# Kernel tuning notes

Hardware: AMD Instinct MI355X
Metric: run time of the kernel (lower is better)

Reference implementation:

```python
import jax, jax.numpy as jnp
import numpy as np

B, S, D_MODEL, D_FF, E, K = 4, 2048, 1024, 4096, 8, 2
CAP_FACTOR = 1.0


def setup_inputs() -> dict:
    key = jax.random.key(0)
    ks = jax.random.split(key, 6)
    std = 0.02
    return {
        "x": jax.random.normal(ks[0], (B, S, D_MODEL), jnp.float32),
        "router_w": jax.random.normal(ks[1], (E, D_MODEL), jnp.float32) * std,  # Linear(d_model,E,bias=False) weight
        "w1": jax.random.normal(ks[2], (E, D_MODEL, D_FF), jnp.float32) * std,
        "b1": jnp.zeros((E, D_FF), jnp.float32),
        "w2": jax.random.normal(ks[3], (E, D_FF, D_MODEL), jnp.float32) * std,
        "b2": jnp.zeros((E, D_MODEL), jnp.float32),
    }


def reference(x, router_w, w1, b1, w2, b2):
    b, s, d = x.shape
    T = b * s
    e = router_w.shape[0]
    capacity = int(CAP_FACTOR * T / e)  # static
    xf = x.reshape(T, d)

    # --- routing ---
    logits = xf @ router_w.T                       # [T,E]
    probs = jax.nn.softmax(logits, axis=-1)
    vals, idx = jax.lax.top_k(probs, K)            # [T,K] values / expert ids
    vals = vals / vals.sum(-1, keepdims=True)

    # dense gate matrix [T,E]; top_k experts are distinct so this is a scatter of K weights per token
    ar = jnp.arange(T)
    gates = jnp.zeros((T, e), x.dtype).at[ar[:, None], idx].add(vals)

    # --- load-balancing loss ---
    counts = jnp.zeros((e,), jnp.float32).at[idx.reshape(-1)].add(1.0)
    ideal = T * K / e
    lb_loss = jnp.sum((counts - ideal) ** 2) / (T ** 2)

    # --- capacity-limited dispatch (first `capacity` tokens in token order per expert) ---
    mask = gates > 0                                               # [T,E]
    order = jnp.argsort(jnp.logical_not(mask), axis=0)[:capacity]  # stable: assigned tokens first, ascending token id -> [cap,E]
    valid = jnp.take_along_axis(mask, order, axis=0)               # [cap,E] token actually assigned & within capacity
    idx_ec = order.T                                               # [E,cap]

    # --- grouped expert MLP ---
    xg = xf[idx_ec]                                                # [E,cap,D]
    h = jax.nn.gelu(jnp.einsum('ecd,edf->ecf', xg, w1) + b1[:, None, :], approximate=False)
    y = jnp.einsum('ecf,efd->ecd', h, w2) + b2[:, None, :]         # [E,cap,D]

    # --- combine (scatter-add with routing weights; dropped/invalid slots get weight 0) ---
    wt = gates[idx_ec, jnp.arange(e)[:, None]] * valid.T           # [E,cap]
    out = jnp.zeros((T, d), x.dtype).at[idx_ec.reshape(-1)].add((y * wt[..., None]).reshape(-1, d))
    return out.reshape(b, s, d), lb_loss
```

## Files before the change

kernel.cpp:

```cpp
#include <hip/hip_runtime.h>
#include <hip/hip_bf16.h>

#define T_TOK 8192
#define DMODEL 1024
#define DFF 4096
#define NEXP 8
#define CAP 1024

typedef __attribute__((ext_vector_type(8))) __bf16 bf16x8;
typedef __attribute__((ext_vector_type(4))) float f32x4;

__device__ __forceinline__ unsigned short f2bf(float f) {
  union { float f; unsigned int u; } v;
  v.f = f;
  return (unsigned short)((v.u + 0x7fffu + ((v.u >> 16) & 1u)) >> 16);
}

__device__ __forceinline__ float fast_gelu(float v) {
  float x = fabsf(v) * 0.70710678118654752440f;
  float t = __builtin_amdgcn_rcpf(1.0f + 0.3275911f * x);
  float poly = t * (0.254829592f + t * (-0.284496736f + t * (1.421413741f +
               t * (-1.453152027f + t * 1.061405429f))));
  float er = 1.0f - poly * __expf(-x * x);
  float s = (v >= 0.0f) ? er : -er;
  return 0.5f * v * (1.0f + s);
}

__device__ __forceinline__ void load_lds16(const unsigned short* g, unsigned short* l) {
  __builtin_amdgcn_global_load_lds((const __attribute__((address_space(1))) void*)g,
                                   (__attribute__((address_space(3))) void*)l,
                                   16, 0, 0);
}

__global__ void k_router(const float* __restrict__ x, const float* __restrict__ rw,
                         unsigned short* __restrict__ xb,
                         int* __restrict__ tk_idx, float* __restrict__ tk_w) {
  int wv = threadIdx.x >> 6, lane = threadIdx.x & 63;
  int t = blockIdx.x * 4 + wv;
  const float4* xr = (const float4*)(x + (size_t)t * DMODEL);
  uint2* xbw = (uint2*)(xb + (size_t)t * DMODEL);
  float acc[NEXP];
#pragma unroll
  for (int e = 0; e < NEXP; ++e) acc[e] = 0.f;
#pragma unroll
  for (int j = 0; j < DMODEL / 256; ++j) {
    float4 v = xr[j * 64 + lane];
#pragma unroll
    for (int e = 0; e < NEXP; ++e) {
      float4 w = ((const float4*)(rw + e * DMODEL))[j * 64 + lane];
      acc[e] += v.x * w.x + v.y * w.y + v.z * w.z + v.w * w.w;
    }
    uint2 p;
    p.x = (unsigned int)f2bf(v.x) | ((unsigned int)f2bf(v.y) << 16);
    p.y = (unsigned int)f2bf(v.z) | ((unsigned int)f2bf(v.w) << 16);
    xbw[j * 64 + lane] = p;
  }
#pragma unroll
  for (int e = 0; e < NEXP; ++e)
    for (int off = 32; off; off >>= 1) acc[e] += __shfl_xor(acc[e], off);
  if (lane == 0) {
    int i0 = 0;
    for (int e = 1; e < NEXP; ++e) if (acc[e] > acc[i0]) i0 = e;
    int i1 = (i0 == 0) ? 1 : 0;
    for (int e = 0; e < NEXP; ++e) if (e != i0 && acc[e] > acc[i1]) i1 = e;
    float ex = expf(acc[i1] - acc[i0]);
    float w0 = 1.f / (1.f + ex);
    float w1 = ex / (1.f + ex);
    tk_idx[2 * t] = i0; tk_idx[2 * t + 1] = i1;
    tk_w[2 * t] = w0;  tk_w[2 * t + 1] = w1;
  }
}

__global__ void k_transpose_cvt(const float* __restrict__ src, unsigned short* __restrict__ dst,
                                int Kd, int Nd) {
  __shared__ unsigned short tile[64][73];
  int e = blockIdx.z;
  size_t k0 = (size_t)blockIdx.y * 64, n0 = (size_t)blockIdx.x * 64;
  int tid = threadIdx.x;
  const float* sb = src + (size_t)e * Kd * Nd;
  int r = tid >> 4, cg = (tid & 15) * 4;
  for (int rr = 0; rr < 4; ++rr) {
    int row = r + rr * 16;
    float4 v = *(const float4*)(sb + (k0 + row) * Nd + n0 + cg);
    tile[row][cg + 0] = f2bf(v.x);
    tile[row][cg + 1] = f2bf(v.y);
    tile[row][cg + 2] = f2bf(v.z);
    tile[row][cg + 3] = f2bf(v.w);
  }
  __syncthreads();
  unsigned short* db = dst + (size_t)e * Nd * Kd;
  int rn = tid >> 3, kg = (tid & 7) * 8;
  for (int rr = 0; rr < 2; ++rr) {
    int nrow = rn + rr * 32;
    union { unsigned short h[8]; uint4 v; } o;
#pragma unroll
    for (int j = 0; j < 8; ++j) o.h[j] = tile[kg + j][nrow];
    *(uint4*)(db + (n0 + nrow) * Kd + k0 + kg) = o.v;
  }
}

__global__ void k_scan(const int* __restrict__ tk_idx, const float* __restrict__ tk_w,
                       int* __restrict__ etok, float* __restrict__ egate,
                       float* __restrict__ loss_out) {
  __shared__ int wavecnt[16][NEXP];
  __shared__ int waveoff[16][NEXP];
  __shared__ int offs[NEXP];
  __shared__ int ctot[NEXP];
  int tid = threadIdx.x;
  int lane = tid & 63, wv = tid >> 6;
  if (tid < NEXP) offs[tid] = 0;
  for (int i = tid; i < NEXP * CAP; i += 1024) { etok[i] = 0; egate[i] = 0.f; }
  __syncthreads();
  unsigned long long lt = (1ULL << lane) - 1ULL;
  for (int c = 0; c < T_TOK / 1024; ++c) {
    int t = c * 1024 + tid;
    int e0 = tk_idx[2 * t], e1 = tk_idx[2 * t + 1];
    float w0 = tk_w[2 * t], w1 = tk_w[2 * t + 1];
    int p0 = 0, p1 = 0;
#pragma unroll
    for (int e = 0; e < NEXP; ++e) {
      unsigned long long bal = __ballot((e0 == e) || (e1 == e));
      if (e0 == e) p0 = __popcll(bal & lt);
      if (e1 == e) p1 = __popcll(bal & lt);
      if (lane == 0) wavecnt[wv][e] = __popcll(bal);
    }
    __syncthreads();
    if (tid < NEXP) {
      int s = 0;
      for (int w = 0; w < 16; ++w) { waveoff[w][tid] = s; s += wavecnt[w][tid]; }
      ctot[tid] = s;
    }
    __syncthreads();
    int r0 = offs[e0] + waveoff[wv][e0] + p0;
    int r1 = offs[e1] + waveoff[wv][e1] + p1;
    if (r0 < CAP) { etok[e0 * CAP + r0] = t; egate[e0 * CAP + r0] = w0; }
    if (r1 < CAP) { etok[e1 * CAP + r1] = t; egate[e1 * CAP + r1] = w1; }
    __syncthreads();
    if (tid < NEXP) offs[tid] += ctot[tid];
    __syncthreads();
  }
  if (tid == 0) {
    float loss = 0.f;
    for (int e = 0; e < NEXP; ++e) {
      float d = (float)offs[e] - 2048.0f;
      loss += d * d;
    }
    loss_out[0] = loss / (8192.0f * 8192.0f);
  }
}

__global__ __launch_bounds__(256) void k_gemm1(
    const unsigned short* __restrict__ xb, const unsigned short* __restrict__ w1t,
    const float* __restrict__ b1, const int* __restrict__ etok,
    unsigned short* __restrict__ H) {
  __shared__ __align__(16) unsigned short smem[8192];
  unsigned short* As = smem;
  unsigned short* Bs = smem + 4096;
  int tid = threadIdx.x;
  int lane = tid & 63, wv = tid >> 6;
  int bid = blockIdx.x;
  int e = bid >> 8;
  int b = bid & 255;
  int nl = b & 7, m = (b >> 3) & 7, nh = b >> 6;
  int m0 = m * 128, n0 = (nh * 8 + nl) * 128;

  const unsigned short* gA[2];
  const unsigned short* gB[2];
  unsigned short* lA[2];
  unsigned short* lB[2];
#pragma unroll
  for (int s = 0; s < 2; ++s) {
    int i = s * 256 + tid;
    int row = i >> 2, cb = (i & 3) * 8;
    int tok = etok[e * CAP + m0 + row];
    gA[s] = xb + (size_t)tok * DMODEL + cb;
    gB[s] = w1t + ((size_t)e * DFF + n0 + row) * DMODEL + cb;
    int wb = (s * 256 + wv * 64) * 8;
    lA[s] = As + wb;
    lB[s] = Bs + wb;
  }

  f32x4 zero = {0.f, 0.f, 0.f, 0.f};
  f32x4 acc[4][4];
#pragma unroll
  for (int mi = 0; mi < 4; ++mi)
#pragma unroll
    for (int ni = 0; ni < 4; ++ni) acc[mi][ni] = zero;

  int wm = (wv >> 1) * 64, wn = (wv & 1) * 64;
  int fr = lane & 15, quad = lane >> 4;
  const unsigned short* pa = As + (wm + fr) * 32 + quad * 8;
  const unsigned short* pb = Bs + (wn + fr) * 32 + quad * 8;

  for (int k0 = 0; k0 < DMODEL; k0 += 32) {
#pragma unroll
    for (int s = 0; s < 2; ++s) {
      load_lds16(gA[s] + k0, lA[s]);
      load_lds16(gB[s] + k0, lB[s]);
    }
    __syncthreads();
    bf16x8 av[4], bv[4];
#pragma unroll
    for (int mi = 0; mi < 4; ++mi) av[mi] = *(const bf16x8*)(pa + mi * 16 * 32);
#pragma unroll
    for (int ni = 0; ni < 4; ++ni) bv[ni] = *(const bf16x8*)(pb + ni * 16 * 32);
#pragma unroll
    for (int mi = 0; mi < 4; ++mi)
#pragma unroll
      for (int ni = 0; ni < 4; ++ni)
        acc[mi][ni] = __builtin_amdgcn_mfma_f32_16x16x32_bf16(bv[ni], av[mi], acc[mi][ni], 0, 0, 0);
    __syncthreads();
  }

  unsigned short* EP = smem + wv * 1536;
#pragma unroll
  for (int ni = 0; ni < 4; ++ni) {
    float4 b4 = *(const float4*)(b1 + e * DFF + n0 + wn + ni * 16 + quad * 4);
#pragma unroll
    for (int mi = 0; mi < 4; ++mi) {
      float v0 = fast_gelu(acc[mi][ni][0] + b4.x);
      float v1 = fast_gelu(acc[mi][ni][1] + b4.y);
      float v2 = fast_gelu(acc[mi][ni][2] + b4.z);
      float v3 = fast_gelu(acc[mi][ni][3] + b4.w);
      uint2 p;
      p.x = (unsigned int)f2bf(v0) | ((unsigned int)f2bf(v1) << 16);
      p.y = (unsigned int)f2bf(v2) | ((unsigned int)f2bf(v3) << 16);
      *(uint2*)(EP + (mi * 16 + fr) * 24 + quad * 4) = p;
    }
#pragma unroll
    for (int t = 0; t < 2; ++t) {
      int row = t * 32 + (lane >> 1), chunk = lane & 1;
      uint4 v = *(const uint4*)(EP + row * 24 + chunk * 8);
      *(uint4*)(H + ((size_t)e * CAP + m0 + wm + row) * DFF + n0 + wn + ni * 16 + chunk * 8) = v;
    }
  }
}

__global__ __launch_bounds__(256) void k_gemm2(
    const unsigned short* __restrict__ H, const unsigned short* __restrict__ w2t,
    const float* __restrict__ b2, const int* __restrict__ etok,
    const float* __restrict__ egate, float* __restrict__ out) {
  __shared__ __align__(16) unsigned short smem[8192];
  unsigned short* As = smem;
  unsigned short* Bs = smem + 4096;
  int tid = threadIdx.x;
  int lane = tid & 63, wv = tid >> 6;
  int bid = blockIdx.x;
  int e = bid >> 7;
  int ks = (bid >> 6) & 1;
  int m0 = ((bid >> 3) & 7) * 128;
  int n0 = (bid & 7) * 128;
  int kbase = ks * (DFF / 2);

  const unsigned short* gA[2];
  const unsigned short* gB[2];
  unsigned short* lA[2];
  unsigned short* lB[2];
#pragma unroll
  for (int s = 0; s < 2; ++s) {
    int i = s * 256 + tid;
    int row = i >> 2, cb = (i & 3) * 8;
    gA[s] = H + ((size_t)e * CAP + m0 + row) * DFF + kbase + cb;
    gB[s] = w2t + ((size_t)e * DMODEL + n0 + row) * DFF + kbase + cb;
    int wb = (s * 256 + wv * 64) * 8;
    lA[s] = As + wb;
    lB[s] = Bs + wb;
  }

  f32x4 zero = {0.f, 0.f, 0.f, 0.f};
  f32x4 acc[4][4];
#pragma unroll
  for (int mi = 0; mi < 4; ++mi)
#pragma unroll
    for (int ni = 0; ni < 4; ++ni) acc[mi][ni] = zero;

  int wm = (wv >> 1) * 64, wn = (wv & 1) * 64;
  int fr = lane & 15, quad = lane >> 4;
  const unsigned short* pa = As + (wm + fr) * 32 + quad * 8;
  const unsigned short* pb = Bs + (wn + fr) * 32 + quad * 8;

  for (int k0 = 0; k0 < DFF / 2; k0 += 32) {
#pragma unroll
    for (int s = 0; s < 2; ++s) {
      load_lds16(gA[s] + k0, lA[s]);
      load_lds16(gB[s] + k0, lB[s]);
    }
    __syncthreads();
    bf16x8 av[4], bv[4];
#pragma unroll
    for (int mi = 0; mi < 4; ++mi) av[mi] = *(const bf16x8*)(pa + mi * 16 * 32);
#pragma unroll
    for (int ni = 0; ni < 4; ++ni) bv[ni] = *(const bf16x8*)(pb + ni * 16 * 32);
#pragma unroll
    for (int mi = 0; mi < 4; ++mi)
#pragma unroll
      for (int ni = 0; ni < 4; ++ni)
        acc[mi][ni] = __builtin_amdgcn_mfma_f32_16x16x32_bf16(av[mi], bv[ni], acc[mi][ni], 0, 0, 0);
    __syncthreads();
  }

  float bs[4];
  int cols[4];
#pragma unroll
  for (int ni = 0; ni < 4; ++ni) {
    cols[ni] = n0 + wn + ni * 16 + fr;
    bs[ni] = (ks == 0) ? b2[e * DMODEL + cols[ni]] : 0.0f;
  }
#pragma unroll
  for (int mi = 0; mi < 4; ++mi) {
    int mbase = m0 + wm + mi * 16 + quad * 4;
#pragma unroll
    for (int rr = 0; rr < 4; ++rr) {
      int mrow = mbase + rr;
      int tok = etok[e * CAP + mrow];
      float g = egate[e * CAP + mrow];
      if (g != 0.f) {
        float* orow = out + (size_t)tok * DMODEL;
#pragma unroll
        for (int ni = 0; ni < 4; ++ni)
          atomicAdd(orow + cols[ni], g * (acc[mi][ni][rr] + bs[ni]));
      }
    }
  }
}

extern "C" void kernel_launch(void* const* d_in, const int* in_sizes, int n_in,
                              void* d_out, int out_size, void* d_ws, size_t ws_size,
                              hipStream_t stream) {
  (void)in_sizes; (void)n_in; (void)ws_size;
  const float* x  = (const float*)d_in[0];
  const float* rw = (const float*)d_in[1];
  const float* w1 = (const float*)d_in[2];
  const float* b1 = (const float*)d_in[3];
  const float* w2 = (const float*)d_in[4];
  const float* b2 = (const float*)d_in[5];
  float* out = (float*)d_out;

  char* ws = (char*)d_ws;
  const size_t XB_BYTES = (size_t)T_TOK * DMODEL * 2;
  const size_t WT_BYTES = (size_t)NEXP * DFF * DMODEL * 2;
  const size_t H_BYTES  = (size_t)NEXP * CAP * DFF * 2;
  unsigned short* xb = (unsigned short*)ws;
  unsigned short* wT = (unsigned short*)(ws + XB_BYTES);
  unsigned short* Hb = (unsigned short*)(ws + XB_BYTES + WT_BYTES);
  char* small = ws + XB_BYTES + WT_BYTES + H_BYTES;
  int*   etok  = (int*)small;
  float* egate = (float*)(small + NEXP * CAP * 4);
  int*   tkidx = (int*)(small + 2 * NEXP * CAP * 4);
  float* tkw   = (float*)(small + 2 * NEXP * CAP * 4 + T_TOK * 2 * 4);

  hipMemsetAsync(d_out, 0, (size_t)out_size * sizeof(float), stream);
  k_router<<<T_TOK / 4, 256, 0, stream>>>(x, rw, xb, tkidx, tkw);
  k_scan<<<1, 1024, 0, stream>>>(tkidx, tkw, etok, egate,
                                 (float*)d_out + (size_t)T_TOK * DMODEL);
  k_transpose_cvt<<<dim3(DFF / 64, DMODEL / 64, NEXP), 256, 0, stream>>>(w1, wT, DMODEL, DFF);
  k_gemm1<<<NEXP * 256, 256, 0, stream>>>(xb, wT, b1, etok, Hb);
  k_transpose_cvt<<<dim3(DMODEL / 64, DFF / 64, NEXP), 256, 0, stream>>>(w2, wT, DFF, DMODEL);
  k_gemm2<<<NEXP * 128, 256, 0, stream>>>(Hb, wT, b2, etok, egate, out);
}
```

Measured before the change: 610.4 us.

## Replace atomic scatter combine with bf16 expert outputs and inverse-index gather

The second grouped GEMM no longer splits K in two or scatters into the output with float atomics. It now runs the full K loop, adds the bias and writes bf16 expert outputs to a staging buffer. A new combine kernel gathers each token's two expert rows through an inverse slot map built during the scan and writes the output once, which also removes the output memset. The scan is parallelised to one block per expert. In exchange, gemm2 launches half as many blocks, each with twice the K work, which lowers occupancy, and Y is rounded to bf16 before combining.

```diff
diff --git a/kernel.cpp b/kernel.cpp
--- a/kernel.cpp
+++ b/kernel.cpp
@@ -14,6 +14,10 @@
   union { float f; unsigned int u; } v;
   v.f = f;
   return (unsigned short)((v.u + 0x7fffu + ((v.u >> 16) & 1u)) >> 16);
+}
+
+__device__ __forceinline__ float bfbits2f(unsigned int lo16) {
+  union { unsigned int u; float f; } v; v.u = lo16 << 16; return v.f;
 }
 
 __device__ __forceinline__ float fast_gelu(float v) {
@@ -34,7 +38,9 @@
 
 __global__ void k_router(const float* __restrict__ x, const float* __restrict__ rw,
                          unsigned short* __restrict__ xb,
-                         int* __restrict__ tk_idx, float* __restrict__ tk_w) {
+                         int* __restrict__ tk_idx, float* __restrict__ tk_w,
+                         int* __restrict__ tinv) {
+  if (threadIdx.x < 8) tinv[blockIdx.x * 8 + threadIdx.x] = -1;
   int wv = threadIdx.x >> 6, lane = threadIdx.x & 63;
   int t = blockIdx.x * 4 + wv;
   const float4* xr = (const float4*)(x + (size_t)t * DMODEL);
@@ -101,52 +107,41 @@
 
 __global__ void k_scan(const int* __restrict__ tk_idx, const float* __restrict__ tk_w,
                        int* __restrict__ etok, float* __restrict__ egate,
-                       float* __restrict__ loss_out) {
-  __shared__ int wavecnt[16][NEXP];
-  __shared__ int waveoff[16][NEXP];
-  __shared__ int offs[NEXP];
-  __shared__ int ctot[NEXP];
-  int tid = threadIdx.x;
-  int lane = tid & 63, wv = tid >> 6;
-  if (tid < NEXP) offs[tid] = 0;
-  for (int i = tid; i < NEXP * CAP; i += 1024) { etok[i] = 0; egate[i] = 0.f; }
+                       int* __restrict__ tinv, int* __restrict__ counts) {
+  __shared__ int wavecnt[16], waveoff[16];
+  __shared__ int soff;
+  int e = blockIdx.x;
+  int tid = threadIdx.x, lane = tid & 63, wv = tid >> 6;
+  for (int i = tid; i < CAP; i += 1024) etok[e * CAP + i] = 0;
+  if (tid == 0) soff = 0;
   __syncthreads();
   unsigned long long lt = (1ULL << lane) - 1ULL;
   for (int c = 0; c < T_TOK / 1024; ++c) {
     int t = c * 1024 + tid;
     int e0 = tk_idx[2 * t], e1 = tk_idx[2 * t + 1];
-    float w0 = tk_w[2 * t], w1 = tk_w[2 * t + 1];
-    int p0 = 0, p1 = 0;
-#pragma unroll
-    for (int e = 0; e < NEXP; ++e) {
-      unsigned long long bal = __ballot((e0 == e) || (e1 == e));
-      if (e0 == e) p0 = __popcll(bal & lt);
-      if (e1 == e) p1 = __popcll(bal & lt);
-      if (lane == 0) wavecnt[wv][e] = __popcll(bal);
-    }
-    __syncthreads();
-    if (tid < NEXP) {
-      int s = 0;
-      for (int w = 0; w < 16; ++w) { waveoff[w][tid] = s; s += wavecnt[w][tid]; }
-      ctot[tid] = s;
-    }
-    __syncthreads();
-    int r0 = offs[e0] + waveoff[wv][e0] + p0;
-    int r1 = offs[e1] + waveoff[wv][e1] + p1;
-    if (r0 < CAP) { etok[e0 * CAP + r0] = t; egate[e0 * CAP + r0] = w0; }
-    if (r1 < CAP) { etok[e1 * CAP + r1] = t; egate[e1 * CAP + r1] = w1; }
-    __syncthreads();
-    if (tid < NEXP) offs[tid] += ctot[tid];
-    __syncthreads();
-  }
-  if (tid == 0) {
-    float loss = 0.f;
-    for (int e = 0; e < NEXP; ++e) {
-      float d = (float)offs[e] - 2048.0f;
-      loss += d * d;
-    }
-    loss_out[0] = loss / (8192.0f * 8192.0f);
-  }
+    bool is0 = (e0 == e), is1 = (e1 == e);
+    bool mine = is0 || is1;
+    unsigned long long bal = __ballot(mine);
+    int pos = __popcll(bal & lt);
+    if (lane == 0) wavecnt[wv] = __popcll(bal);
+    __syncthreads();
+    if (tid == 0) {
+      int s = soff;
+      for (int w = 0; w < 16; ++w) { waveoff[w] = s; s += wavecnt[w]; }
+      soff = s;
+    }
+    __syncthreads();
+    if (mine) {
+      int r = waveoff[wv] + pos;
+      if (r < CAP) {
+        etok[e * CAP + r] = t;
+        egate[e * CAP + r] = is0 ? tk_w[2 * t] : tk_w[2 * t + 1];
+        tinv[2 * t + (is1 ? 1 : 0)] = e * CAP + r;
+      }
+    }
+    __syncthreads();
+  }
+  if (tid == 0) counts[e] = soff;
 }
 
 __global__ __launch_bounds__(256) void k_gemm1(
@@ -238,19 +233,16 @@
 
 __global__ __launch_bounds__(256) void k_gemm2(
     const unsigned short* __restrict__ H, const unsigned short* __restrict__ w2t,
-    const float* __restrict__ b2, const int* __restrict__ etok,
-    const float* __restrict__ egate, float* __restrict__ out) {
+    const float* __restrict__ b2, unsigned short* __restrict__ Y) {
   __shared__ __align__(16) unsigned short smem[8192];
   unsigned short* As = smem;
   unsigned short* Bs = smem + 4096;
   int tid = threadIdx.x;
   int lane = tid & 63, wv = tid >> 6;
   int bid = blockIdx.x;
-  int e = bid >> 7;
-  int ks = (bid >> 6) & 1;
+  int e = bid >> 6;
   int m0 = ((bid >> 3) & 7) * 128;
   int n0 = (bid & 7) * 128;
-  int kbase = ks * (DFF / 2);
 
   const unsigned short* gA[2];
   const unsigned short* gB[2];
@@ -260,8 +252,8 @@
   for (int s = 0; s < 2; ++s) {
     int i = s * 256 + tid;
     int row = i >> 2, cb = (i & 3) * 8;
-    gA[s] = H + ((size_t)e * CAP + m0 + row) * DFF + kbase + cb;
-    gB[s] = w2t + ((size_t)e * DMODEL + n0 + row) * DFF + kbase + cb;
+    gA[s] = H + ((size_t)e * CAP + m0 + row) * DFF + cb;
+    gB[s] = w2t + ((size_t)e * DMODEL + n0 + row) * DFF + cb;
     int wb = (s * 256 + wv * 64) * 8;
     lA[s] = As + wb;
     lB[s] = Bs + wb;
@@ -279,7 +271,7 @@
   const unsigned short* pa = As + (wm + fr) * 32 + quad * 8;
   const unsigned short* pb = Bs + (wn + fr) * 32 + quad * 8;
 
-  for (int k0 = 0; k0 < DFF / 2; k0 += 32) {
+  for (int k0 = 0; k0 < DFF; k0 += 32) {
 #pragma unroll
     for (int s = 0; s < 2; ++s) {
       load_lds16(gA[s] + k0, lA[s]);
@@ -295,39 +287,69 @@
     for (int mi = 0; mi < 4; ++mi)
 #pragma unroll
       for (int ni = 0; ni < 4; ++ni)
-        acc[mi][ni] = __builtin_amdgcn_mfma_f32_16x16x32_bf16(av[mi], bv[ni], acc[mi][ni], 0, 0, 0);
-    __syncthreads();
-  }
-
-  float bs[4];
-  int cols[4];
+        acc[mi][ni] = __builtin_amdgcn_mfma_f32_16x16x32_bf16(bv[ni], av[mi], acc[mi][ni], 0, 0, 0);
+    __syncthreads();
+  }
+
+  unsigned short* EP = smem + wv * 1536;
 #pragma unroll
   for (int ni = 0; ni < 4; ++ni) {
-    cols[ni] = n0 + wn + ni * 16 + fr;
-    bs[ni] = (ks == 0) ? b2[e * DMODEL + cols[ni]] : 0.0f;
-  }
-#pragma unroll
-  for (int mi = 0; mi < 4; ++mi) {
-    int mbase = m0 + wm + mi * 16 + quad * 4;
-#pragma unroll
-    for (int rr = 0; rr < 4; ++rr) {
-      int mrow = mbase + rr;
-      int tok = etok[e * CAP + mrow];
-      float g = egate[e * CAP + mrow];
-      if (g != 0.f) {
-        float* orow = out + (size_t)tok * DMODEL;
-#pragma unroll
-        for (int ni = 0; ni < 4; ++ni)
-          atomicAdd(orow + cols[ni], g * (acc[mi][ni][rr] + bs[ni]));
-      }
-    }
+    float4 b4 = *(const float4*)(b2 + e * DMODEL + n0 + wn + ni * 16 + quad * 4);
+#pragma unroll
+    for (int mi = 0; mi < 4; ++mi) {
+      uint2 p;
+      p.x = (unsigned int)f2bf(acc[mi][ni][0] + b4.x) |
+            ((unsigned int)f2bf(acc[mi][ni][1] + b4.y) << 16);
+      p.y = (unsigned int)f2bf(acc[mi][ni][2] + b4.z) |
+            ((unsigned int)f2bf(acc[mi][ni][3] + b4.w) << 16);
+      *(uint2*)(EP + (mi * 16 + fr) * 24 + quad * 4) = p;
+    }
+#pragma unroll
+    for (int t = 0; t < 2; ++t) {
+      int row = t * 32 + (lane >> 1), chunk = lane & 1;
+      uint4 v = *(const uint4*)(EP + row * 24 + chunk * 8);
+      *(uint4*)(Y + ((size_t)e * CAP + m0 + wm + row) * DMODEL + n0 + wn + ni * 16 + chunk * 8) = v;
+    }
+  }
+}
+
+__global__ void k_combine(const unsigned short* __restrict__ Y,
+                          const float* __restrict__ egate,
+                          const int* __restrict__ tinv,
+                          const int* __restrict__ counts,
+                          float* __restrict__ out, float* __restrict__ loss_out) {
+  int t = blockIdx.x, tid = threadIdx.x;
+  int s0 = tinv[2 * t], s1 = tinv[2 * t + 1];
+  int d0 = tid * 4;
+  float a0 = 0.f, a1 = 0.f, a2 = 0.f, a3 = 0.f;
+  if (s0 >= 0) {
+    float g = egate[s0];
+    uint2 v = *(const uint2*)(Y + (size_t)s0 * DMODEL + d0);
+    a0 += g * bfbits2f(v.x & 0xffff); a1 += g * bfbits2f(v.x >> 16);
+    a2 += g * bfbits2f(v.y & 0xffff); a3 += g * bfbits2f(v.y >> 16);
+  }
+  if (s1 >= 0) {
+    float g = egate[s1];
+    uint2 v = *(const uint2*)(Y + (size_t)s1 * DMODEL + d0);
+    a0 += g * bfbits2f(v.x & 0xffff); a1 += g * bfbits2f(v.x >> 16);
+    a2 += g * bfbits2f(v.y & 0xffff); a3 += g * bfbits2f(v.y >> 16);
+  }
+  float4 o = {a0, a1, a2, a3};
+  *(float4*)(out + (size_t)t * DMODEL + d0) = o;
+  if (t == 0 && tid == 0) {
+    float loss = 0.f;
+    for (int e = 0; e < NEXP; ++e) {
+      float d = (float)counts[e] - 2048.0f;
+      loss += d * d;
+    }
+    loss_out[0] = loss / (8192.0f * 8192.0f);
   }
 }
 
 extern "C" void kernel_launch(void* const* d_in, const int* in_sizes, int n_in,
                               void* d_out, int out_size, void* d_ws, size_t ws_size,
                               hipStream_t stream) {
-  (void)in_sizes; (void)n_in; (void)ws_size;
+  (void)in_sizes; (void)n_in; (void)ws_size; (void)out_size;
   const float* x  = (const float*)d_in[0];
   const float* rw = (const float*)d_in[1];
   const float* w1 = (const float*)d_in[2];
@@ -341,20 +363,23 @@
   const size_t WT_BYTES = (size_t)NEXP * DFF * DMODEL * 2;
   const size_t H_BYTES  = (size_t)NEXP * CAP * DFF * 2;
   unsigned short* xb = (unsigned short*)ws;
+  unsigned short* Yb = xb;
   unsigned short* wT = (unsigned short*)(ws + XB_BYTES);
   unsigned short* Hb = (unsigned short*)(ws + XB_BYTES + WT_BYTES);
   char* small = ws + XB_BYTES + WT_BYTES + H_BYTES;
-  int*   etok  = (int*)small;
-  float* egate = (float*)(small + NEXP * CAP * 4);
-  int*   tkidx = (int*)(small + 2 * NEXP * CAP * 4);
-  float* tkw   = (float*)(small + 2 * NEXP * CAP * 4 + T_TOK * 2 * 4);
-
-  hipMemsetAsync(d_out, 0, (size_t)out_size * sizeof(float), stream);
-  k_router<<<T_TOK / 4, 256, 0, stream>>>(x, rw, xb, tkidx, tkw);
-  k_scan<<<1, 1024, 0, stream>>>(tkidx, tkw, etok, egate,
-                                 (float*)d_out + (size_t)T_TOK * DMODEL);
+  int*   etok   = (int*)small;
+  float* egate  = (float*)(small + NEXP * CAP * 4);
+  int*   tkidx  = (int*)(small + 2 * NEXP * CAP * 4);
+  float* tkw    = (float*)(small + 2 * NEXP * CAP * 4 + T_TOK * 2 * 4);
+  int*   tinv   = (int*)(small + 2 * NEXP * CAP * 4 + 2 * T_TOK * 2 * 4);
+  int*   counts = (int*)(small + 2 * NEXP * CAP * 4 + 3 * T_TOK * 2 * 4);
+
+  k_router<<<T_TOK / 4, 256, 0, stream>>>(x, rw, xb, tkidx, tkw, tinv);
+  k_scan<<<NEXP, 1024, 0, stream>>>(tkidx, tkw, etok, egate, tinv, counts);
   k_transpose_cvt<<<dim3(DFF / 64, DMODEL / 64, NEXP), 256, 0, stream>>>(w1, wT, DMODEL, DFF);
   k_gemm1<<<NEXP * 256, 256, 0, stream>>>(xb, wT, b1, etok, Hb);
   k_transpose_cvt<<<dim3(DMODEL / 64, DFF / 64, NEXP), 256, 0, stream>>>(w2, wT, DFF, DMODEL);
-  k_gemm2<<<NEXP * 128, 256, 0, stream>>>(Hb, wT, b2, etok, egate, out);
-}
+  k_gemm2<<<NEXP * 64, 256, 0, stream>>>(Hb, wT, b2, Yb);
+  k_combine<<<T_TOK, 256, 0, stream>>>(Yb, egate, tinv, counts, out,
+                                       out + (size_t)T_TOK * DMODEL);
+}
```

After: 558.5 us. -8.5%, faster.
